# Performance work log

Hardware: AMD Instinct MI355X
Metric: run time of the kernel (lower is better)

Reference implementation:

```python
import jax, jax.numpy as jnp
import numpy as np

B, S, D, H = 2, 1024, 768, 12
HD = D // H          # head_dim = 64
DFF = 4 * D          # 3072
EPS = 1e-5


def _ln(x, g, b):
    m = x.mean(-1, keepdims=True)
    v = ((x - m) ** 2).mean(-1, keepdims=True)
    return (x - m) * jax.lax.rsqrt(v + EPS) * g + b


def setup_inputs() -> dict:
    key = jax.random.key(0)
    ks = jax.random.split(key, 8)
    w = lambda k, shape: jax.random.normal(k, shape, jnp.float32) * 0.02
    return {
        "inp": jax.random.normal(ks[0], (B, S, D), jnp.float32),
        "attention_mask": jnp.zeros((B, S), bool),  # True = masked out (filled with -inf)
        "rel_matrix": jax.random.randint(ks[1], (B, S, S), -1, 2, jnp.int32),  # values in {-1,0,1}
        "qkv_w": w(ks[2], (3 * D, D)),
        "rel_A": w(ks[3], (3, HD)),        # relative_position_emb_A.weight
        "o_w": w(ks[4], (D, D)),
        "w1": w(ks[5], (DFF, D)), "b1": jnp.zeros((DFF,), jnp.float32),
        "w2": w(ks[6], (D, DFF)), "b2": jnp.zeros((D,), jnp.float32),
        "ln1_g": jnp.ones((D,), jnp.float32), "ln1_b": jnp.zeros((D,), jnp.float32),
        "ln2_g": jnp.ones((D,), jnp.float32), "ln2_b": jnp.zeros((D,), jnp.float32),
    }


def reference(inp, attention_mask, rel_matrix, qkv_w, rel_A, o_w,
              w1, b1, w2, b2, ln1_g, ln1_b, ln2_g, ln2_b):
    x = _ln(inp, ln1_g, ln1_b)
    qkv = x @ qkv_w.T                                  # (B,S,3D)
    q, k, v = jnp.split(qkv, 3, axis=-1)
    heads = lambda t: t.reshape(B, S, H, HD).transpose(0, 2, 1, 3)  # (B,H,S,HD)
    q, k, v = heads(q), heads(k), heads(v)

    # q @ (k + rel_emb)^T without materializing k_aug:
    # q.k^T term plus per-(q,key) relative term gathered from q @ A^T.
    logits = jnp.einsum("bhqd,bhkd->bhqk", q, k)       # (B,H,S,S)
    r = jnp.einsum("bhqd,cd->bhqc", q, rel_A)          # (B,H,S,3)
    idx = (rel_matrix + 1).astype(jnp.int32)           # (B,S,S) in {0,1,2}
    rel = jnp.take_along_axis(r, jnp.broadcast_to(idx[:, None], (B, H, S, S)), axis=-1)
    logits = (logits + rel) / np.sqrt(HD).astype(np.float32)
    # masked_fill: -inf where mask is True
    logits = jnp.where(attention_mask[:, None, None, :], -jnp.inf, logits)

    attn = jax.nn.softmax(logits, axis=-1)
    out = jnp.einsum("bhqk,bhkd->bhqd", attn, v)
    out = out.transpose(0, 2, 1, 3).reshape(B, S, D)
    inp = inp + out @ o_w.T                            # residual (dropout=0)

    h = _ln(inp, ln2_g, ln2_b)
    mlp = jax.nn.relu(h @ w1.T + b1) @ w2.T + b2
    return inp + mlp
```

## Files before the change

### kernel.cpp

```cpp
#include <hip/hip_runtime.h>
#include <hip/hip_bf16.h>

#define BB 2
#define SS 1024
#define DD 768
#define HH 12
#define HD 64
#define DFF 3072
#define EPS 1e-5f
#define BS2 (BB * SS)
#define BSD ((size_t)BS2 * DD)

typedef unsigned short ushort_t;
typedef unsigned char uchar_t;
using short8 = __attribute__((ext_vector_type(8))) short;
using f32x4  = __attribute__((ext_vector_type(4))) float;

#define WAITCNT_LGKM0 0xC07F

__device__ __forceinline__ ushort_t f2bf_rne(float f) {
    union { float f; unsigned u; } x; x.f = f;
    unsigned r = x.u + 0x7fff + ((x.u >> 16) & 1);
    return (ushort_t)(r >> 16);
}
__device__ __forceinline__ float bf2f(short u) {
    union { unsigned i; float f; } x;
    x.i = ((unsigned)(ushort_t)u) << 16;
    return x.f;
}
__device__ __forceinline__ short8 mergeo(short8 a, short8 b, float inv) {
    short8 o;
#pragma unroll
    for (int i = 0; i < 8; ++i)
        o[i] = (short)f2bf_rne((bf2f(a[i]) + bf2f(b[i])) * inv);
    return o;
}

__device__ __forceinline__ void cvt_quad(const float* __restrict__ src, int off,
                                         ushort_t* __restrict__ dst, int i) {
    float4 v = ((const float4*)src)[off];
    ushort4 o;
    o.x = f2bf_rne(v.x); o.y = f2bf_rne(v.y);
    o.z = f2bf_rne(v.z); o.w = f2bf_rne(v.w);
    ((ushort4*)dst)[i] = o;
}

#define P1_CVT (3 * DD * DD / 4 / 256)
#define P1_LN  BS2

__global__ __launch_bounds__(256) void prep1_kernel(
    const float* __restrict__ qkv_w, ushort_t* __restrict__ qkvw_bf,
    const float* __restrict__ x, const float* __restrict__ g,
    const float* __restrict__ b, ushort_t* __restrict__ y)
{
    const int bx = blockIdx.x;
    const int t  = threadIdx.x;
    if (bx < P1_CVT) {
        int i = bx * 256 + t;
        cvt_quad(qkv_w, i, qkvw_bf, i);
        return;
    }
    const int row = bx - P1_CVT;
    const float* xr = x + (size_t)row * DD;
    float s = 0.f, ss = 0.f;
    for (int i = t; i < DD; i += 256) {
        float v = xr[i];
        s += v; ss += v * v;
    }
    for (int off = 32; off; off >>= 1) {
        s  += __shfl_down(s,  off);
        ss += __shfl_down(ss, off);
    }
    __shared__ float reds[4], redss[4], bc[2];
    if ((t & 63) == 0) { reds[t >> 6] = s; redss[t >> 6] = ss; }
    __syncthreads();
    if (t == 0) {
        float S1 = reds[0] + reds[1] + reds[2] + reds[3];
        float S2 = redss[0] + redss[1] + redss[2] + redss[3];
        float mean = S1 / DD;
        float var = S2 / DD - mean * mean;
        bc[0] = mean;
        bc[1] = rsqrtf(var + EPS);
    }
    __syncthreads();
    float mean = bc[0], inv = bc[1];
    ushort_t* yr = y + (size_t)row * DD;
    for (int i = t; i < DD; i += 256) {
        yr[i] = f2bf_rne((xr[i] - mean) * inv * g[i] + b[i]);
    }
}

__global__ __launch_bounds__(256) void merge2_ln_kernel(
    const ushort_t* __restrict__ part, const float* __restrict__ inp,
    const float* __restrict__ g, const float* __restrict__ b,
    float* __restrict__ resid, ushort_t* __restrict__ h_bf)
{
    const int row = blockIdx.x;
    const int t = threadIdx.x;
    float4 v = make_float4(0.f, 0.f, 0.f, 0.f);
    const size_t idx = (size_t)row * (DD / 4) + t;
    if (t < DD / 4) {
        v = ((const float4*)inp)[idx];
        ushort4 p0 = ((const ushort4*)part)[idx];
        ushort4 p1 = ((const ushort4*)(part + BSD))[idx];
        v.x += bf2f(p0.x) + bf2f(p1.x);
        v.y += bf2f(p0.y) + bf2f(p1.y);
        v.z += bf2f(p0.z) + bf2f(p1.z);
        v.w += bf2f(p0.w) + bf2f(p1.w);
        ((float4*)resid)[idx] = v;
    }
    float s  = v.x + v.y + v.z + v.w;
    float ss = v.x * v.x + v.y * v.y + v.z * v.z + v.w * v.w;
    for (int off = 32; off; off >>= 1) {
        s  += __shfl_down(s,  off);
        ss += __shfl_down(ss, off);
    }
    __shared__ float reds[4], redss[4], bc[2];
    if ((t & 63) == 0) { reds[t >> 6] = s; redss[t >> 6] = ss; }
    __syncthreads();
    if (t == 0) {
        float S1 = reds[0] + reds[1] + reds[2] + reds[3];
        float S2 = redss[0] + redss[1] + redss[2] + redss[3];
        float mean = S1 / DD;
        float var = S2 / DD - mean * mean;
        bc[0] = mean;
        bc[1] = rsqrtf(var + EPS);
    }
    __syncthreads();
    if (t < DD / 4) {
        const float mean = bc[0], inv = bc[1];
        float4 gv = ((const float4*)g)[t];
        float4 bv = ((const float4*)b)[t];
        ushort4 o;
        o.x = f2bf_rne((v.x - mean) * inv * gv.x + bv.x);
        o.y = f2bf_rne((v.y - mean) * inv * gv.y + bv.y);
        o.z = f2bf_rne((v.z - mean) * inv * gv.z + bv.z);
        o.w = f2bf_rne((v.w - mean) * inv * gv.w + bv.w);
        ((ushort4*)h_bf)[idx] = o;
    }
}

__global__ __launch_bounds__(256) void merge4_kernel(
    const ushort_t* __restrict__ part, const float* __restrict__ resid,
    const float* __restrict__ b2, float* __restrict__ outp, int n4)
{
    int i = blockIdx.x * 256 + threadIdx.x;
    if (i >= n4) return;
    float4 v = ((const float4*)resid)[i];
    int col4 = (i * 4) % DD;
    float4 bv = *(const float4*)(b2 + col4);
    v.x += bv.x; v.y += bv.y; v.z += bv.z; v.w += bv.w;
#pragma unroll
    for (int z = 0; z < 4; ++z) {
        ushort4 pz = ((const ushort4*)(part + (size_t)z * BSD))[i];
        v.x += bf2f(pz.x); v.y += bf2f(pz.y);
        v.z += bf2f(pz.z); v.w += bf2f(pz.w);
    }
    ((float4*)outp)[i] = v;
}

template <bool RELU, bool OUT_BF16, bool HAS_BIAS, bool PARTIAL, bool FUSE_ATT>
__device__ __forceinline__ void gemm_body(
    int bid, int nwg,
    const ushort_t* __restrict__ A, const ushort_t* __restrict__ W,
    const float* __restrict__ bias, void* __restrict__ Cout,
    const float* __restrict__ lpart,
    int M, int N, int K, int Ksplit, int nx)
{
    __shared__ __align__(16) ushort_t As[512 * 8];
    __shared__ __align__(16) ushort_t Bs[1024 * 8];

    const int swz = (bid & 7) * (nwg >> 3) + (bid >> 3);
    const int by  = swz & 31;
    const int t2  = swz >> 5;
    const int bxx = t2 % nx;
    const int bz  = t2 / nx;

    const int t  = threadIdx.x;
    const int n0 = bxx * 128;
    const int m0 = by * 64;
    const int kb = bz * Ksplit;
    const int w  = t >> 6;
    const int l  = t & 63;
    const int wm = (w & 1) * 32;
    const int wn = (w >> 1) * 64;
    const int l15  = l & 15;
    const int quad = l >> 4;

    const ushort_t* gA = A + (size_t)(m0 + (t & 63)) * K + kb + (t >> 6) * 8;
    const ushort_t* gB = W + (size_t)(n0 + (t & 127)) * K + kb + (t >> 7) * 8;

    const float* lp0 = nullptr; const float* lp1 = nullptr;
    const int hbase = kb >> 6;
    if (FUSE_ATT) {
        lp0 = lpart + (size_t)(m0 + (t & 63)) * HH;
        lp1 = lp0 + (size_t)BS2 * HH;
    }

    short8 pa0, pa1, ra0, ra1, sa0, sa1;
    float li0 = 0.f, li1 = 0.f;
    if (FUSE_ATT) {
        ra0 = *(const short8*)(gA);
        ra1 = *(const short8*)(gA + 32);
        sa0 = *(const short8*)(gA + BSD);
        sa1 = *(const short8*)(gA + BSD + 32);
        li0 = lp0[hbase];
        li1 = lp1[hbase];
    } else {
        pa0 = *(const short8*)(gA);
        pa1 = *(const short8*)(gA + 32);
    }
    short8 pb0 = *(const short8*)(gB);
    short8 pb1 = *(const short8*)(gB + 16);
    short8 pb2 = *(const short8*)(gB + 32);
    short8 pb3 = *(const short8*)(gB + 48);

    f32x4 acc[2][4] = {};
    const int nIter = Ksplit >> 6;

    for (int it = 0; it < nIter; ++it) {
        __builtin_amdgcn_s_barrier();
        if (FUSE_ATT) {
            const float inv = 1.0f / (li0 + li1);
            pa0 = mergeo(ra0, sa0, inv);
            pa1 = mergeo(ra1, sa1, inv);
        }
        *(short8*)&As[(size_t)t * 8]           = pa0;
        *(short8*)&As[(size_t)(t + 256) * 8]   = pa1;
        *(short8*)&Bs[(size_t)t * 8]           = pb0;
        *(short8*)&Bs[(size_t)(t + 256) * 8]   = pb1;
        *(short8*)&Bs[(size_t)(t + 512) * 8]   = pb2;
        *(short8*)&Bs[(size_t)(t + 768) * 8]   = pb3;
        if (it + 1 < nIter) {
            const int k0 = (it + 1) << 6;
            if (FUSE_ATT) {
                ra0 = *(const short8*)(gA + k0);
                ra1 = *(const short8*)(gA + k0 + 32);
                sa0 = *(const short8*)(gA + k0 + BSD);
                sa1 = *(const short8*)(gA + k0 + BSD + 32);
                li0 = lp0[hbase + it + 1];
                li1 = lp1[hbase + it + 1];
            } else {
                pa0 = *(const short8*)(gA + k0);
                pa1 = *(const short8*)(gA + k0 + 32);
            }
            pb0 = *(const short8*)(gB + k0);
            pb1 = *(const short8*)(gB + k0 + 16);
            pb2 = *(const short8*)(gB + k0 + 32);
            pb3 = *(const short8*)(gB + k0 + 48);
        }
        __builtin_amdgcn_s_waitcnt(WAITCNT_LGKM0);
        __builtin_amdgcn_s_barrier();

#pragma unroll
        for (int ks = 0; ks < 2; ++ks) {
            const ushort_t* aptr = &As[(size_t)((ks * 4 + quad) * 64 + wm + l15) * 8];
            const ushort_t* bptr = &Bs[(size_t)((ks * 4 + quad) * 128 + wn + l15) * 8];
            short8 af[2], bf[4];
#pragma unroll
            for (int i = 0; i < 2; ++i)
                af[i] = *(const short8*)(aptr + (size_t)i * 16 * 8);
#pragma unroll
            for (int j = 0; j < 4; ++j)
                bf[j] = *(const short8*)(bptr + (size_t)j * 16 * 8);
#pragma unroll
            for (int i = 0; i < 2; ++i)
#pragma unroll
                for (int j = 0; j < 4; ++j)
                    acc[i][j] = __builtin_amdgcn_mfma_f32_16x16x32_bf16(
                        af[i], bf[j], acc[i][j], 0, 0, 0);
        }
    }

    if (PARTIAL) {
        ushort_t* Cp = (ushort_t*)Cout + (size_t)bz * ((size_t)M * N);
#pragma unroll
        for (int i = 0; i < 2; ++i) {
            const int row = m0 + wm + i * 16 + quad * 4;
#pragma unroll
            for (int j = 0; j < 4; ++j) {
                const int col = n0 + wn + j * 16 + l15;
#pragma unroll
                for (int r = 0; r < 4; ++r)
                    Cp[(size_t)(row + r) * N + col] = f2bf_rne(acc[i][j][r]);
            }
        }
    } else {
#pragma unroll
        for (int i = 0; i < 2; ++i) {
            const int row = m0 + wm + i * 16 + quad * 4;
#pragma unroll
            for (int j = 0; j < 4; ++j) {
                const int col = n0 + wn + j * 16 + l15;
                const float bv = HAS_BIAS ? bias[col] : 0.f;
#pragma unroll
                for (int r = 0; r < 4; ++r) {
                    float v = acc[i][j][r] + bv;
                    if (RELU) v = fmaxf(v, 0.f);
                    if (OUT_BF16)
                        ((ushort_t*)Cout)[(size_t)(row + r) * N + col] = f2bf_rne(v);
                    else
                        ((float*)Cout)[(size_t)(row + r) * N + col] = v;
                }
            }
        }
    }
}

template <bool RELU, bool OUT_BF16, bool HAS_BIAS, bool PARTIAL, bool FUSE_ATT>
__global__ __launch_bounds__(256) void gemm_tile(
    const ushort_t* __restrict__ A, const ushort_t* __restrict__ W,
    const float* __restrict__ bias, void* __restrict__ Cout,
    const float* __restrict__ lpart,
    int M, int N, int K, int Ksplit, int nx)
{
    gemm_body<RELU, OUT_BF16, HAS_BIAS, PARTIAL, FUSE_ATT>(
        blockIdx.x, gridDim.x, A, W, bias, Cout, lpart, M, N, K, Ksplit, nx);
}

#define QKV_G (3 * DD / 128 * 32)

__global__ __launch_bounds__(256) void qkv_codes_kernel(
    const ushort_t* __restrict__ A, const ushort_t* __restrict__ W,
    ushort_t* __restrict__ Cout,
    const int* __restrict__ rel, const uchar_t* __restrict__ mask,
    unsigned* __restrict__ codes)
{
    const int bx = blockIdx.x;
    if (bx < QKV_G) {
        gemm_body<false, true, false, false, false>(
            bx, QKV_G, A, W, nullptr, Cout, nullptr,
            BS2, 3 * DD, DD, DD, 3 * DD / 128);
        return;
    }
    const int t = threadIdx.x;
    int tid = (bx - QKV_G) * 256 + t;
    int l15 = tid & 15;
    int kt  = (tid >> 4) & 15;
    int q   = (tid >> 8) & (SS - 1);
    int bb  = tid >> 18;
    const int* rrow = rel + ((size_t)(bb * SS + q)) * SS + kt * 64 + l15;
    const uchar_t* mrow = mask + (size_t)bb * SS + kt * 64 + l15;
    unsigned o = 0;
#pragma unroll
    for (int nt = 0; nt < 4; ++nt) {
        unsigned c = mrow[nt * 16] ? 3u : (unsigned)(rrow[nt * 16] + 1);
        o |= c << (8 * nt);
    }
    codes[((size_t)(bb * SS + q) * 16 + kt) * 16 + l15] = o;
}

#define ATT_G (BB * HH * 16 * 2)
#define RC1 (DD * DD / 4)
#define RC2 (RC1 + DFF * DD / 4)
#define RCT (RC2 + DD * DFF / 4)
#define RCVT_BLK (RCT / 256)

__global__ __launch_bounds__(256) void attn_cvt_kernel(
    const ushort_t* __restrict__ qkv,
    const unsigned* __restrict__ codes,
    const float* __restrict__ rel_A,
    ushort_t* __restrict__ Opart,
    float* __restrict__ lpart,
    const float* __restrict__ o_w, const float* __restrict__ w1,
    const float* __restrict__ w2, ushort_t* __restrict__ wrest)
{
    const int bx = blockIdx.x;
    const int t  = threadIdx.x;
    if (bx >= ATT_G) {
        int i = (bx - ATT_G) * 256 + t;
        const float* src; int off;
        if (i < RC1)      { src = o_w; off = i; }
        else if (i < RC2) { src = w1;  off = i - RC1; }
        else              { src = w2;  off = i - RC2; }
        cvt_quad(src, off, wrest, i);
        return;
    }

    __shared__ __align__(16) ushort_t Ks[2][64 * 64];
    __shared__ __align__(16) unsigned Vt2[2][64 * 36];
    __shared__ __align__(16) ushort_t Ps[64 * 72];
    __shared__ __align__(16) float r3s[64][4];

    const int ks = bx & 1;
    const int qt = (bx >> 1) & 15;
    const int h  = (bx >> 5) % HH;
    const int b  = bx / (32 * HH);
    const int q0 = qt * 64;
    const int w  = t >> 6;
    const int l  = t & 63;
    const int l15  = l & 15;
    const int quad = l >> 4;

    const int sr  = t >> 3;
    const int scp = t & 7;
    const int vkp = t >> 3;
    const int vdg = t & 7;
    const int vkps = vkp ^ (vdg * 4);

    const size_t qrow = (size_t)(b * SS + q0 + w * 16 + l15) * (3 * DD) + h * HD;
    const short8 qf0 = *(const short8*)(qkv + qrow + quad * 8);
    const short8 qf1 = *(const short8*)(qkv + qrow + 32 + quad * 8);

    {
        float rv[3];
#pragma unroll
        for (int c = 0; c < 3; ++c) {
            const float* a = rel_A + c * HD + quad * 8;
            float acc = 0.f;
#pragma unroll
            for (int j = 0; j < 8; ++j) acc += bf2f(qf0[j]) * a[j];
#pragma unroll
            for (int j = 0; j < 8; ++j) acc += bf2f(qf1[j]) * a[32 + j];
            acc += __shfl_xor(acc, 16);
            acc += __shfl_xor(acc, 32);
            rv[c] = acc;
        }
        if (quad == 0) {
            float4 f4 = make_float4(rv[0], rv[1], rv[2], -2.4e31f);
            *(float4*)&r3s[w * 16 + l15][0] = f4;
        }
    }

    float l_run[4] = {0.f, 0.f, 0.f, 0.f};
    f32x4 oacc[4] = {};

    const int kt0 = ks * 8;
    short8 va, vb;
    {
        const int k0 = kt0 * 64;
        const int cl  = scp ^ (sr & 7);
        const ushort_t* g = qkv + (size_t)(b * SS + k0 + sr) * (3 * DD) + DD + h * HD + cl * 8;
        __builtin_amdgcn_global_load_lds(
            (const __attribute__((address_space(1))) unsigned*)g,
            (__attribute__((address_space(3))) unsigned*)(&Ks[0][0] + (size_t)t * 8), 16, 0, 0);
        const int r2  = sr + 32;
        const int cl2 = scp ^ (r2 & 7);
        const ushort_t* g2 = qkv + (size_t)(b * SS + k0 + r2) * (3 * DD) + DD + h * HD + cl2 * 8;
        __builtin_amdgcn_global_load_lds(
            (const __attribute__((address_space(1))) unsigned*)g2,
            (__attribute__((address_space(3))) unsigned*)(&Ks[0][0] + (size_t)(t + 256) * 8), 16, 0, 0);
        const ushort_t* gv = qkv + (size_t)(b * SS + k0 + 2 * vkp) * (3 * DD) + 2 * DD + h * HD + vdg * 8;
        va = *(const short8*)gv;
        vb = *(const short8*)(gv + 3 * DD);
#pragma unroll
        for (int i = 0; i < 8; ++i)
            Vt2[0][(size_t)(vdg * 8 + i) * 36 + vkps] =
                (unsigned)(ushort_t)va[i] | ((unsigned)(ushort_t)vb[i] << 16);
    }
    __syncthreads();
    float4 r3v[4];
#pragma unroll
    for (int reg = 0; reg < 4; ++reg)
        r3v[reg] = *(const float4*)&r3s[w * 16 + quad * 4 + reg][0];

    for (int i8 = 0; i8 < 8; ++i8) {
        const int kt  = kt0 + i8;
        const int cur = i8 & 1;
        const bool more = (i8 + 1 < 8);
        if (more) {
            const int k0 = (kt + 1) * 64;
            const int nb = cur ^ 1;
            const int cl  = scp ^ (sr & 7);
            const ushort_t* g = qkv + (size_t)(b * SS + k0 + sr) * (3 * DD) + DD + h * HD + cl * 8;
            __builtin_amdgcn_global_load_lds(
                (const __attribute__((address_space(1))) unsigned*)g,
                (__attribute__((address_space(3))) unsigned*)(&Ks[nb][0] + (size_t)t * 8), 16, 0, 0);
            const int r2  = sr + 32;
            const int cl2 = scp ^ (r2 & 7);
            const ushort_t* g2 = qkv + (size_t)(b * SS + k0 + r2) * (3 * DD) + DD + h * HD + cl2 * 8;
            __builtin_amdgcn_global_load_lds(
                (const __attribute__((address_space(1))) unsigned*)g2,
                (__attribute__((address_space(3))) unsigned*)(&Ks[nb][0] + (size_t)(t + 256) * 8), 16, 0, 0);
            const ushort_t* gv = qkv + (size_t)(b * SS + k0 + 2 * vkp) * (3 * DD) + 2 * DD + h * HD + vdg * 8;
            va = *(const short8*)gv;
            vb = *(const short8*)(gv + 3 * DD);
        }

        f32x4 sacc[4] = {};
#pragma unroll
        for (int kc = 0; kc < 2; ++kc) {
            const short8 qv = kc ? qf1 : qf0;
#pragma unroll
            for (int nt = 0; nt < 4; ++nt) {
                const int row = nt * 16 + l15;
                const int cp  = (kc * 4 + quad) ^ (row & 7);
                const short8 kf = *(const short8*)(&Ks[cur][0] + (size_t)row * 64 + cp * 8);
                sacc[nt] = __builtin_amdgcn_mfma_f32_16x16x32_bf16(qv, kf, sacc[nt], 0, 0, 0);
            }
        }

#pragma unroll
        for (int reg = 0; reg < 4; ++reg) {
            const int qloc = w * 16 + quad * 4 + reg;
            const unsigned cds = codes[((size_t)(b * SS + q0 + qloc) * 16 + kt) * 16 + l15];
            const float4 r4 = r3v[reg];
#pragma unroll
            for (int nt = 0; nt < 4; ++nt) {
                const unsigned c = (cds >> (8 * nt)) & 0xff;
                float rvv = (c == 0) ? r4.x : (c == 1) ? r4.y : (c == 2) ? r4.z : r4.w;
                const float p = __expf((sacc[nt][reg] + rvv) * 0.125f);
                l_run[reg] += p;
                Ps[(size_t)qloc * 72 + nt * 16 + l15] = f2bf_rne(p);
            }
        }

#pragma unroll
        for (int kc = 0; kc < 2; ++kc) {
            const short8 pf = *(const short8*)(Ps + (size_t)(w * 16 + l15) * 72 + kc * 32 + quad * 8);
#pragma unroll
            for (int dt = 0; dt < 4; ++dt) {
                const int d  = dt * 16 + l15;
                const int dg = d >> 3;
                const int kps0 = (kc * 16 + quad * 4) ^ ((dg & 7) * 4);
                const short8 vf = *(const short8*)((const ushort_t*)&Vt2[cur][(size_t)d * 36 + kps0]);
                oacc[dt] = __builtin_amdgcn_mfma_f32_16x16x32_bf16(pf, vf, oacc[dt], 0, 0, 0);
            }
        }

        if (more) {
            const int nb = cur ^ 1;
#pragma unroll
            for (int i = 0; i < 8; ++i)
                Vt2[nb][(size_t)(vdg * 8 + i) * 36 + vkps] =
                    (unsigned)(ushort_t)va[i] | ((unsigned)(ushort_t)vb[i] << 16);
            __syncthreads();
        }
    }

    ushort_t* Op = Opart + (size_t)ks * BSD;
    float* lp = lpart + (size_t)ks * BS2 * HH;
#pragma unroll
    for (int reg = 0; reg < 4; ++reg) {
        float ls = l_run[reg];
        ls += __shfl_xor(ls, 1);
        ls += __shfl_xor(ls, 2);
        ls += __shfl_xor(ls, 4);
        ls += __shfl_xor(ls, 8);
        const int orow = b * SS + q0 + w * 16 + quad * 4 + reg;
#pragma unroll
        for (int dt = 0; dt < 4; ++dt)
            Op[(size_t)orow * DD + h * HD + dt * 16 + l15] = f2bf_rne(oacc[dt][reg]);
        if (l15 == 0) lp[(size_t)orow * HH + h] = ls;
    }
}

extern "C" void kernel_launch(void* const* d_in, const int* in_sizes, int n_in,
                              void* d_out, int out_size, void* d_ws, size_t ws_size,
                              hipStream_t stream) {
    const float* inp   = (const float*)d_in[0];
    const uchar_t* amask = (const uchar_t*)d_in[1];
    const int*   relm  = (const int*)d_in[2];
    const float* qkv_w = (const float*)d_in[3];
    const float* rel_A = (const float*)d_in[4];
    const float* o_w   = (const float*)d_in[5];
    const float* w1    = (const float*)d_in[6];
    const float* b1    = (const float*)d_in[7];
    const float* w2    = (const float*)d_in[8];
    const float* b2    = (const float*)d_in[9];
    const float* ln1_g = (const float*)d_in[10];
    const float* ln1_b = (const float*)d_in[11];
    const float* ln2_g = (const float*)d_in[12];
    const float* ln2_b = (const float*)d_in[13];
    float* out = (float*)d_out;

    char* p = (char*)d_ws;
    ushort_t* x_bf   = (ushort_t*)p; p += BSD * 2;
    ushort_t* h_bf   = (ushort_t*)p; p += BSD * 2;
    ushort_t* ff_bf  = (ushort_t*)p; p += (size_t)BS2 * DFF * 2;
    ushort_t* qkvw_bf= (ushort_t*)p; p += (size_t)3 * DD * DD * 2;
    ushort_t* ow_bf  = (ushort_t*)p; p += (size_t)DD * DD * 2;
    ushort_t* w1_bf  = (ushort_t*)p; p += (size_t)DFF * DD * 2;
    ushort_t* w2_bf  = (ushort_t*)p; p += (size_t)DD * DFF * 2;
    ushort_t* qkv_bf = (ushort_t*)p; p += (size_t)BS2 * 3 * DD * 2;
    float*    resid  = (float*)p;    p += BSD * 4;
    ushort_t* pool   = (ushort_t*)p; p += 4 * BSD * 2;
    ushort_t* Opart  = (ushort_t*)p; p += 2 * BSD * 2;
    float*    lpart  = (float*)p;    p += (size_t)2 * BS2 * HH * 4;
    unsigned* codes  = (unsigned*)p; p += (size_t)BB * SS * SS;

    prep1_kernel<<<P1_CVT + P1_LN, 256, 0, stream>>>(
        qkv_w, qkvw_bf, inp, ln1_g, ln1_b, x_bf);

    qkv_codes_kernel<<<QKV_G + BB * SS, 256, 0, stream>>>(
        x_bf, qkvw_bf, qkv_bf, relm, amask, codes);

    attn_cvt_kernel<<<ATT_G + RCVT_BLK, 256, 0, stream>>>(
        qkv_bf, codes, rel_A, Opart, lpart, o_w, w1, w2, ow_bf);

    gemm_tile<false, false, false, true, true>
        <<<DD / 128 * 32 * 2, 256, 0, stream>>>(
        Opart, ow_bf, nullptr, pool, lpart, BS2, DD, DD, DD / 2, DD / 128);

    merge2_ln_kernel<<<BS2, 256, 0, stream>>>(
        pool, inp, ln2_g, ln2_b, resid, h_bf);

    gemm_tile<true, true, true, false, false>
        <<<DFF / 128 * 32, 256, 0, stream>>>(
        h_bf, w1_bf, b1, ff_bf, nullptr, BS2, DFF, DD, DD, DFF / 128);

    gemm_tile<false, false, false, true, false>
        <<<DD / 128 * 32 * 4, 256, 0, stream>>>(
        ff_bf, w2_bf, nullptr, pool, nullptr, BS2, DD, DFF, DFF / 4, DD / 128);

    merge4_kernel<<<(int)(BSD / 4 / 256), 256, 0, stream>>>(
        pool, resid, b2, out, (int)(BSD / 4));
}
```

Measured before the change: 253.8 us.

## Use 128x128 double-buffered direct-to-LDS GEMM for QKV and MLP projections

Adds a new GEMM body with 128x128 output tiles, each wave computing 64x64, fed by global_load_lds async copies into double-buffered shared memory with vmcnt-based waits. The QKV, FFN1 and FFN2 GEMMs switch to it, halving block counts, while the attention-fused output projection keeps the old 64x128 register-staged path under a dedicated kernel. This aims for more data reuse per tile and overlap of global loads with MFMA work. The cost is doubled LDS use and more accumulators per thread, which may lower occupancy, and fewer blocks to fill the GPU's many CUs.

```diff
diff --git a/kernel.cpp b/kernel.cpp
--- a/kernel.cpp
+++ b/kernel.cpp
@@ -35,7 +35,6 @@
         o[i] = (short)f2bf_rne((bf2f(a[i]) + bf2f(b[i])) * inv);
     return o;
 }
-
 __device__ __forceinline__ void cvt_quad(const float* __restrict__ src, int off,
                                          ushort_t* __restrict__ dst, int i) {
     float4 v = ((const float4*)src)[off];
@@ -159,12 +158,139 @@
     ((float4*)outp)[i] = v;
 }
 
-template <bool RELU, bool OUT_BF16, bool HAS_BIAS, bool PARTIAL, bool FUSE_ATT>
-__device__ __forceinline__ void gemm_body(
+template <bool RELU, bool OUT_BF16, bool HAS_BIAS, bool PARTIAL>
+__device__ __forceinline__ void gemm128_body(
     int bid, int nwg,
     const ushort_t* __restrict__ A, const ushort_t* __restrict__ W,
     const float* __restrict__ bias, void* __restrict__ Cout,
-    const float* __restrict__ lpart,
+    int M, int N, int K, int Ksplit, int nx)
+{
+    __shared__ __align__(16) ushort_t As[2][1024 * 8];
+    __shared__ __align__(16) ushort_t Bs[2][1024 * 8];
+
+    const int swz = (bid & 7) * (nwg >> 3) + (bid >> 3);
+    const int by  = swz & 15;
+    const int t2  = swz >> 4;
+    const int bxx = t2 % nx;
+    const int bz  = t2 / nx;
+
+    const int t  = threadIdx.x;
+    const int n0 = bxx * 128;
+    const int m0 = by * 128;
+    const int kb = bz * Ksplit;
+    const int w  = t >> 6;
+    const int l  = t & 63;
+    const int wm = (w & 1) * 64;
+    const int wn = (w >> 1) * 64;
+    const int l15  = l & 15;
+    const int quad = l >> 4;
+
+    const int rowT = t & 127;
+    const int kq0  = t >> 7;
+    const ushort_t* gA = A + (size_t)(m0 + rowT) * K + kb + kq0 * 8;
+    const ushort_t* gB = W + (size_t)(n0 + rowT) * K + kb + kq0 * 8;
+
+    auto stage = [&](int buf, int k0) {
+#pragma unroll
+        for (int j = 0; j < 4; ++j) {
+            __builtin_amdgcn_global_load_lds(
+                (const __attribute__((address_space(1))) unsigned*)(gA + k0 + j * 16),
+                (__attribute__((address_space(3))) unsigned*)(&As[buf][(size_t)(j * 256 + t) * 8]),
+                16, 0, 0);
+            __builtin_amdgcn_global_load_lds(
+                (const __attribute__((address_space(1))) unsigned*)(gB + k0 + j * 16),
+                (__attribute__((address_space(3))) unsigned*)(&Bs[buf][(size_t)(j * 256 + t) * 8]),
+                16, 0, 0);
+        }
+    };
+
+    f32x4 acc[4][4] = {};
+    const int nIter = Ksplit >> 6;
+
+    stage(0, 0);
+    stage(1, 64);
+
+    for (int it = 0; it < nIter; ++it) {
+        const int cur = it & 1;
+        if (it + 1 < nIter) {
+            asm volatile("s_waitcnt vmcnt(8)" ::: "memory");
+        } else {
+            asm volatile("s_waitcnt vmcnt(0)" ::: "memory");
+        }
+        __builtin_amdgcn_sched_barrier(0);
+        __builtin_amdgcn_s_barrier();
+
+#pragma unroll
+        for (int ks = 0; ks < 2; ++ks) {
+            const ushort_t* aptr = &As[cur][(size_t)((ks * 4 + quad) * 128 + wm + l15) * 8];
+            const ushort_t* bptr = &Bs[cur][(size_t)((ks * 4 + quad) * 128 + wn + l15) * 8];
+            short8 af[4], bf[4];
+#pragma unroll
+            for (int i = 0; i < 4; ++i)
+                af[i] = *(const short8*)(aptr + (size_t)i * 16 * 8);
+#pragma unroll
+            for (int j = 0; j < 4; ++j)
+                bf[j] = *(const short8*)(bptr + (size_t)j * 16 * 8);
+#pragma unroll
+            for (int i = 0; i < 4; ++i)
+#pragma unroll
+                for (int j = 0; j < 4; ++j)
+                    acc[i][j] = __builtin_amdgcn_mfma_f32_16x16x32_bf16(
+                        af[i], bf[j], acc[i][j], 0, 0, 0);
+        }
+        __builtin_amdgcn_s_barrier();
+        if (it + 2 < nIter) stage(cur, (it + 2) << 6);
+    }
+
+    if (PARTIAL) {
+        ushort_t* Cp = (ushort_t*)Cout + (size_t)bz * ((size_t)M * N);
+#pragma unroll
+        for (int i = 0; i < 4; ++i) {
+            const int row = m0 + wm + i * 16 + quad * 4;
+#pragma unroll
+            for (int j = 0; j < 4; ++j) {
+                const int col = n0 + wn + j * 16 + l15;
+#pragma unroll
+                for (int r = 0; r < 4; ++r)
+                    Cp[(size_t)(row + r) * N + col] = f2bf_rne(acc[i][j][r]);
+            }
+        }
+    } else {
+#pragma unroll
+        for (int i = 0; i < 4; ++i) {
+            const int row = m0 + wm + i * 16 + quad * 4;
+#pragma unroll
+            for (int j = 0; j < 4; ++j) {
+                const int col = n0 + wn + j * 16 + l15;
+                const float bv = HAS_BIAS ? bias[col] : 0.f;
+#pragma unroll
+                for (int r = 0; r < 4; ++r) {
+                    float v = acc[i][j][r] + bv;
+                    if (RELU) v = fmaxf(v, 0.f);
+                    if (OUT_BF16)
+                        ((ushort_t*)Cout)[(size_t)(row + r) * N + col] = f2bf_rne(v);
+                    else
+                        ((float*)Cout)[(size_t)(row + r) * N + col] = v;
+                }
+            }
+        }
+    }
+}
+
+template <bool RELU, bool OUT_BF16, bool HAS_BIAS, bool PARTIAL>
+__global__ __launch_bounds__(256) void gemm128_tile(
+    const ushort_t* __restrict__ A, const ushort_t* __restrict__ W,
+    const float* __restrict__ bias, void* __restrict__ Cout,
+    int M, int N, int K, int Ksplit, int nx)
+{
+    gemm128_body<RELU, OUT_BF16, HAS_BIAS, PARTIAL>(
+        blockIdx.x, gridDim.x, A, W, bias, Cout, M, N, K, Ksplit, nx);
+}
+
+__device__ __forceinline__ void gemm_oproj_body(
+    int bid, int nwg,
+    const ushort_t* __restrict__ A, const ushort_t* __restrict__ W,
+    void* __restrict__ Cout, const float* __restrict__ lpart,
     int M, int N, int K, int Ksplit, int nx)
 {
     __shared__ __align__(16) ushort_t As[512 * 8];
@@ -190,26 +316,17 @@
     const ushort_t* gA = A + (size_t)(m0 + (t & 63)) * K + kb + (t >> 6) * 8;
     const ushort_t* gB = W + (size_t)(n0 + (t & 127)) * K + kb + (t >> 7) * 8;
 
-    const float* lp0 = nullptr; const float* lp1 = nullptr;
     const int hbase = kb >> 6;
-    if (FUSE_ATT) {
-        lp0 = lpart + (size_t)(m0 + (t & 63)) * HH;
-        lp1 = lp0 + (size_t)BS2 * HH;
-    }
+    const float* lp0 = lpart + (size_t)(m0 + (t & 63)) * HH;
+    const float* lp1 = lp0 + (size_t)BS2 * HH;
 
     short8 pa0, pa1, ra0, ra1, sa0, sa1;
-    float li0 = 0.f, li1 = 0.f;
-    if (FUSE_ATT) {
-        ra0 = *(const short8*)(gA);
-        ra1 = *(const short8*)(gA + 32);
-        sa0 = *(const short8*)(gA + BSD);
-        sa1 = *(const short8*)(gA + BSD + 32);
-        li0 = lp0[hbase];
-        li1 = lp1[hbase];
-    } else {
-        pa0 = *(const short8*)(gA);
-        pa1 = *(const short8*)(gA + 32);
-    }
+    ra0 = *(const short8*)(gA);
+    ra1 = *(const short8*)(gA + 32);
+    sa0 = *(const short8*)(gA + BSD);
+    sa1 = *(const short8*)(gA + BSD + 32);
+    float li0 = lp0[hbase];
+    float li1 = lp1[hbase];
     short8 pb0 = *(const short8*)(gB);
     short8 pb1 = *(const short8*)(gB + 16);
     short8 pb2 = *(const short8*)(gB + 32);
@@ -220,7 +337,7 @@
 
     for (int it = 0; it < nIter; ++it) {
         __builtin_amdgcn_s_barrier();
-        if (FUSE_ATT) {
+        {
             const float inv = 1.0f / (li0 + li1);
             pa0 = mergeo(ra0, sa0, inv);
             pa1 = mergeo(ra1, sa1, inv);
@@ -233,17 +350,12 @@
         *(short8*)&Bs[(size_t)(t + 768) * 8]   = pb3;
         if (it + 1 < nIter) {
             const int k0 = (it + 1) << 6;
-            if (FUSE_ATT) {
-                ra0 = *(const short8*)(gA + k0);
-                ra1 = *(const short8*)(gA + k0 + 32);
-                sa0 = *(const short8*)(gA + k0 + BSD);
-                sa1 = *(const short8*)(gA + k0 + BSD + 32);
-                li0 = lp0[hbase + it + 1];
-                li1 = lp1[hbase + it + 1];
-            } else {
-                pa0 = *(const short8*)(gA + k0);
-                pa1 = *(const short8*)(gA + k0 + 32);
-            }
+            ra0 = *(const short8*)(gA + k0);
+            ra1 = *(const short8*)(gA + k0 + 32);
+            sa0 = *(const short8*)(gA + k0 + BSD);
+            sa1 = *(const short8*)(gA + k0 + BSD + 32);
+            li0 = lp0[hbase + it + 1];
+            li1 = lp1[hbase + it + 1];
             pb0 = *(const short8*)(gB + k0);
             pb1 = *(const short8*)(gB + k0 + 16);
             pb2 = *(const short8*)(gB + k0 + 32);
@@ -272,53 +384,29 @@
         }
     }
 
-    if (PARTIAL) {
-        ushort_t* Cp = (ushort_t*)Cout + (size_t)bz * ((size_t)M * N);
-#pragma unroll
-        for (int i = 0; i < 2; ++i) {
-            const int row = m0 + wm + i * 16 + quad * 4;
-#pragma unroll
-            for (int j = 0; j < 4; ++j) {
-                const int col = n0 + wn + j * 16 + l15;
-#pragma unroll
-                for (int r = 0; r < 4; ++r)
-                    Cp[(size_t)(row + r) * N + col] = f2bf_rne(acc[i][j][r]);
-            }
-        }
-    } else {
-#pragma unroll
-        for (int i = 0; i < 2; ++i) {
-            const int row = m0 + wm + i * 16 + quad * 4;
-#pragma unroll
-            for (int j = 0; j < 4; ++j) {
-                const int col = n0 + wn + j * 16 + l15;
-                const float bv = HAS_BIAS ? bias[col] : 0.f;
-#pragma unroll
-                for (int r = 0; r < 4; ++r) {
-                    float v = acc[i][j][r] + bv;
-                    if (RELU) v = fmaxf(v, 0.f);
-                    if (OUT_BF16)
-                        ((ushort_t*)Cout)[(size_t)(row + r) * N + col] = f2bf_rne(v);
-                    else
-                        ((float*)Cout)[(size_t)(row + r) * N + col] = v;
-                }
-            }
-        }
-    }
-}
-
-template <bool RELU, bool OUT_BF16, bool HAS_BIAS, bool PARTIAL, bool FUSE_ATT>
-__global__ __launch_bounds__(256) void gemm_tile(
+    ushort_t* Cp = (ushort_t*)Cout + (size_t)bz * ((size_t)M * N);
+#pragma unroll
+    for (int i = 0; i < 2; ++i) {
+        const int row = m0 + wm + i * 16 + quad * 4;
+#pragma unroll
+        for (int j = 0; j < 4; ++j) {
+            const int col = n0 + wn + j * 16 + l15;
+#pragma unroll
+            for (int r = 0; r < 4; ++r)
+                Cp[(size_t)(row + r) * N + col] = f2bf_rne(acc[i][j][r]);
+        }
+    }
+}
+
+__global__ __launch_bounds__(256) void oproj_kernel(
     const ushort_t* __restrict__ A, const ushort_t* __restrict__ W,
-    const float* __restrict__ bias, void* __restrict__ Cout,
-    const float* __restrict__ lpart,
+    void* __restrict__ Cout, const float* __restrict__ lpart,
     int M, int N, int K, int Ksplit, int nx)
 {
-    gemm_body<RELU, OUT_BF16, HAS_BIAS, PARTIAL, FUSE_ATT>(
-        blockIdx.x, gridDim.x, A, W, bias, Cout, lpart, M, N, K, Ksplit, nx);
-}
-
-#define QKV_G (3 * DD / 128 * 32)
+    gemm_oproj_body(blockIdx.x, gridDim.x, A, W, Cout, lpart, M, N, K, Ksplit, nx);
+}
+
+#define QKV_G (3 * DD / 128 * 16)
 
 __global__ __launch_bounds__(256) void qkv_codes_kernel(
     const ushort_t* __restrict__ A, const ushort_t* __restrict__ W,
@@ -328,9 +416,8 @@
 {
     const int bx = blockIdx.x;
     if (bx < QKV_G) {
-        gemm_body<false, true, false, false, false>(
-            bx, QKV_G, A, W, nullptr, Cout, nullptr,
-            BS2, 3 * DD, DD, DD, 3 * DD / 128);
+        gemm128_body<false, true, false, false>(
+            bx, QKV_G, A, W, nullptr, Cout, BS2, 3 * DD, DD, DD, 3 * DD / 128);
         return;
     }
     const int t = threadIdx.x;
@@ -588,20 +675,19 @@
     attn_cvt_kernel<<<ATT_G + RCVT_BLK, 256, 0, stream>>>(
         qkv_bf, codes, rel_A, Opart, lpart, o_w, w1, w2, ow_bf);
 
-    gemm_tile<false, false, false, true, true>
-        <<<DD / 128 * 32 * 2, 256, 0, stream>>>(
-        Opart, ow_bf, nullptr, pool, lpart, BS2, DD, DD, DD / 2, DD / 128);
+    oproj_kernel<<<DD / 128 * 32 * 2, 256, 0, stream>>>(
+        Opart, ow_bf, pool, lpart, BS2, DD, DD, DD / 2, DD / 128);
 
     merge2_ln_kernel<<<BS2, 256, 0, stream>>>(
         pool, inp, ln2_g, ln2_b, resid, h_bf);
 
-    gemm_tile<true, true, true, false, false>
-        <<<DFF / 128 * 32, 256, 0, stream>>>(
-        h_bf, w1_bf, b1, ff_bf, nullptr, BS2, DFF, DD, DD, DFF / 128);
-
-    gemm_tile<false, false, false, true, false>
-        <<<DD / 128 * 32 * 4, 256, 0, stream>>>(
-        ff_bf, w2_bf, nullptr, pool, nullptr, BS2, DD, DFF, DFF / 4, DD / 128);
+    gemm128_tile<true, true, true, false>
+        <<<DFF / 128 * 16, 256, 0, stream>>>(
+        h_bf, w1_bf, b1, ff_bf, BS2, DFF, DD, DD, DFF / 128);
+
+    gemm128_tile<false, false, false, true>
+        <<<DD / 128 * 16 * 4, 256, 0, stream>>>(
+        ff_bf, w2_bf, nullptr, pool, BS2, DD, DFF, DFF / 4, DD / 128);
 
     merge4_kernel<<<(int)(BSD / 4 / 256), 256, 0, stream>>>(
         pool, resid, b2, out, (int)(BSD / 4));
```

Result: no change. 256.3 us (+1.0%).
